# Performance work log

Hardware: AMD Instinct MI355X
Metric: run time of the kernel (lower is better)

Reference implementation:

```python
import jax, jax.numpy as jnp
import numpy as np

# Hardcoded hyperparameters from the torch module
E = 128   # n_embd
H = 4     # n_head
HS = 32   # head_size = n_embd // n_head
L = 4     # n_layer
T = 512   # block_size (full context)
V = 512   # vocab_size (quantization_levels)
B = 64    # batch
SCALE = 0.02  # init std per _init_weights


def _ln(x, g, b):
    mu = x.mean(-1, keepdims=True)
    var = ((x - mu) ** 2).mean(-1, keepdims=True)
    return (x - mu) / jnp.sqrt(var + 1e-5) * g + b


def setup_inputs() -> dict:
    key = jax.random.key(0)
    ks = jax.random.split(key, 24)
    rn = lambda k, shape: SCALE * jax.random.normal(k, shape, dtype=jnp.float32)
    return {
        "idx": jax.random.randint(ks[0], (B, T), 0, V),
        "tok_emb": rn(ks[1], (V, E)),
        "pos_emb": rn(ks[2], (T, E)),
        # per-head projections, stacked over layers and heads: x[...,E] @ wq[l,h] -> [...,HS]
        "wq": rn(ks[3], (L, H, E, HS)),
        "wk": rn(ks[4], (L, H, E, HS)),
        "wv": rn(ks[5], (L, H, E, HS)),
        "w_proj": rn(ks[6], (L, E, E)),   # torch Linear weight layout [out, in]
        "b_proj": jnp.zeros((L, E), jnp.float32),
        "ln1_g": jnp.ones((L, E), jnp.float32),
        "ln1_b": jnp.zeros((L, E), jnp.float32),
        "ln2_g": jnp.ones((L, E), jnp.float32),
        "ln2_b": jnp.zeros((L, E), jnp.float32),
        "w1": rn(ks[7], (L, 4 * E, E)),
        "b1": jnp.zeros((L, 4 * E), jnp.float32),
        "w2": rn(ks[8], (L, E, 4 * E)),
        "b2": jnp.zeros((L, E), jnp.float32),
        "lnf_g": jnp.ones((E,), jnp.float32),
        "lnf_b": jnp.zeros((E,), jnp.float32),
        "w_head": rn(ks[9], (V, E)),
        "b_head": jnp.zeros((V,), jnp.float32),
    }


def reference(idx, tok_emb, pos_emb, wq, wk, wv, w_proj, b_proj,
              ln1_g, ln1_b, ln2_g, ln2_b, w1, b1, w2, b2,
              lnf_g, lnf_b, w_head, b_head):
    Bv, Tv = idx.shape
    x = tok_emb[idx] + pos_emb[None, :Tv, :]          # [B,T,E]
    causal = jnp.tril(jnp.ones((Tv, Tv), dtype=bool))
    for l in range(L):
        h = _ln(x, ln1_g[l], ln1_b[l])
        q = jnp.einsum('bte,hed->bhtd', h, wq[l])     # [B,H,T,HS]
        k = jnp.einsum('bte,hed->bhtd', h, wk[l])
        v = jnp.einsum('bte,hed->bhtd', h, wv[l])
        s = jnp.einsum('bhtd,bhsd->bhts', q, k) * (HS ** -0.5)
        s = jnp.where(causal, s, -jnp.inf)
        a = jax.nn.softmax(s, axis=-1)
        o = jnp.einsum('bhts,bhsd->bhtd', a, v)       # [B,H,T,HS]
        o = o.transpose(0, 2, 1, 3).reshape(Bv, Tv, E)  # concat heads
        x = x + o @ w_proj[l].T + b_proj[l]
        h = _ln(x, ln2_g[l], ln2_b[l])
        x = x + jax.nn.gelu(h @ w1[l].T + b1[l], approximate=False) @ w2[l].T + b2[l]
    x = _ln(x, lnf_g, lnf_b)
    logits = x @ w_head.T + b_head                    # [B,T,V]
    return logits
```

## Files before the change

kernel.cpp:

```cpp
#include <hip/hip_runtime.h>

typedef __bf16 bf16x8 __attribute__((ext_vector_type(8)));
typedef __bf16 bf16x2 __attribute__((ext_vector_type(2)));
typedef float f32x4 __attribute__((ext_vector_type(4)));

constexpr int E_ = 128, H_ = 4, HS_ = 32, L_ = 4, T_ = 512, V_ = 512, B_ = 64;
constexpr int M_ = B_ * T_;

__device__ __forceinline__ float b2f(ushort u) {
    return __uint_as_float(((uint)u) << 16);
}
__device__ __forceinline__ ushort f2b(float f) {
    uint x = __float_as_uint(f);
    uint r = (x + 0x7fffu + ((x >> 16) & 1u)) >> 16;
    return (ushort)r;
}
__device__ __forceinline__ uint packbf(float a, float b) {
    bf16x2 t; t[0] = (__bf16)a; t[1] = (__bf16)b;
    return __builtin_bit_cast(uint, t);
}

constexpr int kNSeg = 19;
constexpr int kOffs[kNSeg + 1] = {
    0, 65536, 131072, 196608, 262144, 327680, 393216, 393728, 394240, 394752,
    395264, 395776, 657920, 659968, 922112, 922624, 922752, 922880, 988416, 988928
};
constexpr int kTotal = 988928;

struct SrcPtrs { const void* p[kNSeg]; };

__global__ __launch_bounds__(256) void k_convert(SrcPtrs sp, ushort* __restrict__ arena) {
    int gid = blockIdx.x * 256 + threadIdx.x;
    if (gid >= kTotal) return;
    bool isf32 = (((const uint*)sp.p[7])[0] == 0x3F800000u);
    int s = 0;
    #pragma unroll
    for (int i = 1; i < kNSeg; i++) if (gid >= kOffs[i]) s = i;
    int local = gid - kOffs[s];
    ushort v;
    if (isf32) v = f2b(((const float*)sp.p[s])[local]);
    else       v = ((const ushort*)sp.p[s])[local];
    arena[gid] = v;
}

__global__ void k_prep_qkv(const ushort* __restrict__ wq, const ushort* __restrict__ wk,
                           const ushort* __restrict__ wv, ushort* __restrict__ wt) {
    int gid = blockIdx.x * 256 + threadIdx.x;
    if (gid >= L_ * 384 * E_) return;
    int e = gid & 127;
    int n = (gid >> 7) % 384;
    int l = gid / (384 * E_);
    int part = n >> 7, within = n & 127, hh = within >> 5, d = within & 31;
    const ushort* src = part == 0 ? wq : (part == 1 ? wk : wv);
    wt[gid] = src[(((size_t)(l * H_ + hh) * E_) + e) * HS_ + d];
}

__global__ __launch_bounds__(256) void k_embed_ln(const int* __restrict__ idx,
                                                  const ushort* __restrict__ tok,
                                                  const ushort* __restrict__ pos,
                                                  const ushort* __restrict__ g,
                                                  const ushort* __restrict__ beta,
                                                  float* __restrict__ x, ushort* __restrict__ h) {
    int wave = threadIdx.x >> 6, lane = threadIdx.x & 63;
    int row = blockIdx.x * 4 + wave;
    int t = row & (T_ - 1);
    int id = idx[row];
    float v0 = b2f(tok[id * E_ + lane])      + b2f(pos[t * E_ + lane]);
    float v1 = b2f(tok[id * E_ + lane + 64]) + b2f(pos[t * E_ + lane + 64]);
    size_t o = (size_t)row * E_;
    x[o + lane] = v0; x[o + lane + 64] = v1;
    float s = v0 + v1;
    #pragma unroll
    for (int m = 32; m; m >>= 1) s += __shfl_xor(s, m, 64);
    float mu = s * (1.0f / 128.0f);
    float d0 = v0 - mu, d1 = v1 - mu;
    float ss = d0 * d0 + d1 * d1;
    #pragma unroll
    for (int m = 32; m; m >>= 1) ss += __shfl_xor(ss, m, 64);
    float rstd = rsqrtf(ss * (1.0f / 128.0f) + 1e-5f);
    h[o + lane]      = f2b(d0 * rstd * b2f(g[lane])      + b2f(beta[lane]));
    h[o + lane + 64] = f2b(d1 * rstd * b2f(g[lane + 64]) + b2f(beta[lane + 64]));
}

template<int EPI>
__global__ __launch_bounds__(256) void k_gemm(const ushort* __restrict__ A, const ushort* __restrict__ W,
                                              const ushort* __restrict__ bias, void* __restrict__ outp,
                                              void* __restrict__ outp2,
                                              const ushort* __restrict__ lng, const ushort* __restrict__ lnb,
                                              const uint* __restrict__ dtraw, int K, int lda, int ldc) {
    int wid = threadIdx.x >> 6, lane = threadIdx.x & 63;
    int wr = wid >> 1, wc = wid & 1;
    int bm = blockIdx.x, bn = blockIdx.y;
    int r16 = lane & 15, kq = lane >> 4;
    const ushort* Abase = A + (size_t)(bm * 128 + wr * 64 + r16) * lda + kq * 8;
    const ushort* Wbase = W + (size_t)(bn * 128 + wc * 64 + r16) * K + kq * 8;
    bool f32out = false;
    if constexpr (EPI == 1) f32out = (dtraw[0] == 0x3F800000u);
    f32x4 acc[4][4];
    #pragma unroll
    for (int i = 0; i < 4; i++)
        #pragma unroll
        for (int j = 0; j < 4; j++) acc[i][j] = (f32x4)0.0f;
    for (int k0 = 0; k0 < K; k0 += 32) {
        bf16x8 af[4], wf[4];
        #pragma unroll
        for (int mi = 0; mi < 4; mi++)
            af[mi] = *(const bf16x8*)(Abase + (size_t)mi * 16 * lda + k0);
        #pragma unroll
        for (int ni = 0; ni < 4; ni++)
            wf[ni] = *(const bf16x8*)(Wbase + (size_t)ni * 16 * K + k0);
        #pragma unroll
        for (int mi = 0; mi < 4; mi++)
            #pragma unroll
            for (int ni = 0; ni < 4; ni++)
                acc[mi][ni] = __builtin_amdgcn_mfma_f32_16x16x32_bf16(af[mi], wf[ni], acc[mi][ni], 0, 0, 0);
    }
    int orow0 = bm * 128 + wr * 64 + kq * 4;
    int ocol0 = bn * 128 + wc * 64 + r16;
    if constexpr (EPI == 5) {
        __shared__ float lnS[2][128], lnQ[2][128];
        float*  xg = (float*)outp;
        ushort* hg = (ushort*)outp2;
        #pragma unroll
        for (int ni = 0; ni < 4; ni++) {
            int col = ocol0 + ni * 16;
            float bv = b2f(bias[col]);
            #pragma unroll
            for (int mi = 0; mi < 4; mi++) {
                #pragma unroll
                for (int e = 0; e < 4; e++) {
                    size_t gi = (size_t)(orow0 + mi * 16 + e) * 128 + col;
                    float xv = xg[gi] + acc[mi][ni][e] + bv;
                    xg[gi] = xv;
                    acc[mi][ni][e] = xv;
                }
            }
        }
        #pragma unroll
        for (int mi = 0; mi < 4; mi++) {
            #pragma unroll
            for (int e = 0; e < 4; e++) {
                float s = 0.f, q = 0.f;
                #pragma unroll
                for (int ni = 0; ni < 4; ni++) { float v = acc[mi][ni][e]; s += v; q += v * v; }
                #pragma unroll
                for (int mk = 1; mk < 16; mk <<= 1) {
                    s += __shfl_xor(s, mk, 64); q += __shfl_xor(q, mk, 64);
                }
                if (r16 == 0) {
                    int lrow = wr * 64 + mi * 16 + kq * 4 + e;
                    lnS[wc][lrow] = s; lnQ[wc][lrow] = q;
                }
            }
        }
        __syncthreads();
        float gc[4], bc[4];
        #pragma unroll
        for (int ni = 0; ni < 4; ni++) {
            int col = ocol0 + ni * 16;
            gc[ni] = b2f(lng[col]); bc[ni] = b2f(lnb[col]);
        }
        #pragma unroll
        for (int mi = 0; mi < 4; mi++) {
            #pragma unroll
            for (int e = 0; e < 4; e++) {
                int lrow = wr * 64 + mi * 16 + kq * 4 + e;
                float tot = lnS[0][lrow] + lnS[1][lrow];
                float tq  = lnQ[0][lrow] + lnQ[1][lrow];
                float mu  = tot * (1.0f / 128.0f);
                float var = tq * (1.0f / 128.0f) - mu * mu;
                float rstd = rsqrtf(var + 1e-5f);
                size_t grow = (size_t)(bm * 128 + lrow) * 128;
                #pragma unroll
                for (int ni = 0; ni < 4; ni++) {
                    int col = ocol0 + ni * 16;
                    hg[grow + col] = f2b((acc[mi][ni][e] - mu) * rstd * gc[ni] + bc[ni]);
                }
            }
        }
        return;
    }
    if constexpr (EPI == 4) {
        if (bn == 2) {
            ushort* vt = (ushort*)outp2;
            #pragma unroll
            for (int mi = 0; mi < 4; mi++) {
                int row0 = orow0 + mi * 16;
                int bb = row0 >> 9, tt = row0 & 511;
                #pragma unroll
                for (int ni = 0; ni < 4; ni++) {
                    int vd = (ocol0 - 256) + ni * 16;
                    int hh = vd >> 5, dd = vd & 31;
                    ushort4 pk;
                    pk.x = f2b(acc[mi][ni][0]); pk.y = f2b(acc[mi][ni][1]);
                    pk.z = f2b(acc[mi][ni][2]); pk.w = f2b(acc[mi][ni][3]);
                    *(ushort4*)(vt + (((size_t)(bb * 4 + hh) * 32 + dd) << 9) + tt) = pk;
                }
            }
            return;
        }
    }
    #pragma unroll
    for (int mi = 0; mi < 4; mi++) {
        #pragma unroll
        for (int ni = 0; ni < 4; ni++) {
            int col = ocol0 + ni * 16;
            float bv = 0.0f;
            if constexpr (EPI == 1 || EPI == 2) bv = b2f(bias[col]);
            #pragma unroll
            for (int e = 0; e < 4; e++) {
                int row = orow0 + mi * 16 + e;
                float v = acc[mi][ni][e] + bv;
                if constexpr (EPI == 2) v = 0.5f * v * (1.0f + erff(v * 0.70710678118f));
                if constexpr (EPI == 1) {
                    if (f32out) ((float*)outp)[(size_t)row * ldc + col] = v;
                    else        ((ushort*)outp)[(size_t)row * ldc + col] = f2b(v);
                } else {
                    ((ushort*)outp)[(size_t)row * ldc + col] = f2b(v);
                }
            }
        }
    }
}

constexpr float SC_ = 0.2550348637f;

__device__ __forceinline__ bf16x8 scale8(bf16x8 v, float s) {
    bf16x8 r;
    #pragma unroll
    for (int i = 0; i < 8; i++) r[i] = (__bf16)((float)v[i] * s);
    return r;
}

__device__ __forceinline__ bf16x8 relayoutP(const float* p, int r16, int g) {
    uint pk00 = packbf(p[0], p[1]), pk01 = packbf(p[2], p[3]);
    uint pk10 = packbf(p[4], p[5]), pk11 = packbf(p[6], p[7]);
    int ga = ((g & 1) << 5) + r16;
    int gb = ga + 16;
    uint A0 = (uint)__shfl((int)pk00, ga), A1 = (uint)__shfl((int)pk01, ga);
    uint C0 = (uint)__shfl((int)pk00, gb), C1 = (uint)__shfl((int)pk01, gb);
    uint B0 = (uint)__shfl((int)pk10, ga), B1 = (uint)__shfl((int)pk11, ga);
    uint D0 = (uint)__shfl((int)pk10, gb), D1 = (uint)__shfl((int)pk11, gb);
    bool hi2 = g >= 2;
    uint4 pr;
    pr.x = hi2 ? B0 : A0; pr.y = hi2 ? B1 : A1;
    pr.z = hi2 ? D0 : C0; pr.w = hi2 ? D1 : C1;
    return __builtin_bit_cast(bf16x8, pr);
}

__global__ __launch_bounds__(256) void k_attn_proj(const ushort* __restrict__ qk,
                                                   const ushort* __restrict__ vt,
                                                   const ushort* __restrict__ wproj,
                                                   const ushort* __restrict__ bproj,
                                                   const ushort* __restrict__ lng,
                                                   const ushort* __restrict__ lnb,
                                                   float* __restrict__ x,
                                                   ushort* __restrict__ h) {
    __shared__ ushort olds[16 * 128];
    __shared__ float lnS[4][16], lnQ[4][16];
    int lane = threadIdx.x & 63, w = threadIdx.x >> 6;
    int r16 = lane & 15, g = lane >> 4;
    int bid = blockIdx.x;
    int b = (bid & 7) * 8 + ((bid >> 3) >> 5);
    int i = (bid >> 3) & 31;
    int qbase = i * 16, qmax = qbase + 15, myq = qbase + r16;
    const ushort* qkbase = qk + (size_t)b * 512 * 256;
    bf16x8 qf = scale8(*(const bf16x8*)(qkbase + (size_t)(qbase + r16) * 256 + w * 32 + g * 8), SC_);
    const ushort* kptr = qkbase + 128 + w * 32 + g * 8;
    const ushort* vbase = vt + ((size_t)(b * 4 + w) * 32) * 512;

    f32x4 o0 = (f32x4)0.0f, o1 = (f32x4)0.0f;
    float ps = 0.0f;
    for (int j0 = 0; j0 <= qmax; j0 += 32) {
        bf16x8 kf0 = *(const bf16x8*)(kptr + (size_t)(j0 + r16) * 256);
        bf16x8 kf1 = *(const bf16x8*)(kptr + (size_t)(j0 + 16 + r16) * 256);
        bf16x8 vf0 = *(const bf16x8*)(vbase + (size_t)r16 * 512 + j0 + g * 8);
        bf16x8 vf1 = *(const bf16x8*)(vbase + (size_t)(16 + r16) * 512 + j0 + g * 8);
        f32x4 s0 = __builtin_amdgcn_mfma_f32_16x16x32_bf16(kf0, qf, (f32x4)0.0f, 0, 0, 0);
        f32x4 s1 = __builtin_amdgcn_mfma_f32_16x16x32_bf16(kf1, qf, (f32x4)0.0f, 0, 0, 0);
        float p[8];
        #pragma unroll
        for (int e = 0; e < 4; e++) {
            int ja = j0 + 4 * g + e;
            p[e]     = (ja      <= myq) ? exp2f(s0[e]) : 0.0f;
            p[4 + e] = (ja + 16 <= myq) ? exp2f(s1[e]) : 0.0f;
            ps += p[e] + p[4 + e];
        }
        bf16x8 pf = relayoutP(p, r16, g);
        o0 = __builtin_amdgcn_mfma_f32_16x16x32_bf16(vf0, pf, o0, 0, 0, 0);
        o1 = __builtin_amdgcn_mfma_f32_16x16x32_bf16(vf1, pf, o1, 0, 0, 0);
    }
    ps += __shfl_xor(ps, 16, 64);
    ps += __shfl_xor(ps, 32, 64);
    float inv = 1.0f / ps;
    {
        int base = r16 * 256 + w * 64 + g * 8;
        int sw = (r16 & 7) << 4;
        uint2 pk0, pk1;
        pk0.x = packbf(o0[0] * inv, o0[1] * inv); pk0.y = packbf(o0[2] * inv, o0[3] * inv);
        pk1.x = packbf(o1[0] * inv, o1[1] * inv); pk1.y = packbf(o1[2] * inv, o1[3] * inv);
        *(uint2*)((char*)olds + (base ^ sw))        = pk0;
        *(uint2*)((char*)olds + ((base + 32) ^ sw)) = pk1;
    }
    __syncthreads();
    f32x4 a0 = (f32x4)0.0f, a1 = (f32x4)0.0f;
    const ushort* wp0 = wproj + (size_t)(w * 32 + r16) * 128 + g * 8;
    const ushort* wp1 = wp0 + (size_t)16 * 128;
    #pragma unroll
    for (int kk = 0; kk < 4; kk++) {
        int abyte = (r16 * 256 + kk * 64 + g * 16) ^ ((r16 & 7) << 4);
        bf16x8 af = *(const bf16x8*)((const char*)olds + abyte);
        bf16x8 w0 = *(const bf16x8*)(wp0 + kk * 32);
        bf16x8 w1 = *(const bf16x8*)(wp1 + kk * 32);
        a0 = __builtin_amdgcn_mfma_f32_16x16x32_bf16(af, w0, a0, 0, 0, 0);
        a1 = __builtin_amdgcn_mfma_f32_16x16x32_bf16(af, w1, a1, 0, 0, 0);
    }
    int col0 = w * 32 + r16, col1 = col0 + 16;
    float bv0 = b2f(bproj[col0]), bv1 = b2f(bproj[col1]);
    float xv0[4], xv1[4];
    #pragma unroll
    for (int e = 0; e < 4; e++) {
        size_t gi = (size_t)(b * 512 + qbase + g * 4 + e) * 128;
        float v0 = x[gi + col0] + a0[e] + bv0;
        float v1 = x[gi + col1] + a1[e] + bv1;
        x[gi + col0] = v0; x[gi + col1] = v1;
        xv0[e] = v0; xv1[e] = v1;
    }
    #pragma unroll
    for (int e = 0; e < 4; e++) {
        float s = xv0[e] + xv1[e];
        float q = xv0[e] * xv0[e] + xv1[e] * xv1[e];
        #pragma unroll
        for (int mk = 1; mk < 16; mk <<= 1) {
            s += __shfl_xor(s, mk, 64); q += __shfl_xor(q, mk, 64);
        }
        if (r16 == 0) { lnS[w][g * 4 + e] = s; lnQ[w][g * 4 + e] = q; }
    }
    __syncthreads();
    float g0 = b2f(lng[col0]), g1 = b2f(lng[col1]);
    float be0 = b2f(lnb[col0]), be1 = b2f(lnb[col1]);
    #pragma unroll
    for (int e = 0; e < 4; e++) {
        int q = g * 4 + e;
        float tot = lnS[0][q] + lnS[1][q] + lnS[2][q] + lnS[3][q];
        float tq  = lnQ[0][q] + lnQ[1][q] + lnQ[2][q] + lnQ[3][q];
        float mu  = tot * (1.0f / 128.0f);
        float var = tq * (1.0f / 128.0f) - mu * mu;
        float rstd = rsqrtf(var + 1e-5f);
        size_t gr = (size_t)(b * 512 + qbase + q) * 128;
        h[gr + col0] = f2b((xv0[e] - mu) * rstd * g0 + be0);
        h[gr + col1] = f2b((xv1[e] - mu) * rstd * g1 + be1);
    }
}

extern "C" void kernel_launch(void* const* d_in, const int* in_sizes, int n_in,
                              void* d_out, int out_size, void* d_ws, size_t ws_size,
                              hipStream_t stream) {
    const int* idx = (const int*)d_in[0];

    char* ws = (char*)d_ws;
    float*  x     = (float*) (ws + 0);
    ushort* h     = (ushort*)(ws + (16u << 20));
    ushort* wqkvt = (ushort*)(ws + (24u << 20));
    ushort* arena = (ushort*)(ws + (25u << 20));

    ushort* qkv = (ushort*)d_out;
    ushort* vt  = (ushort*)d_out + (12u << 20);
    ushort* mid = (ushort*)d_out;

    const ushort* tok    = arena + kOffs[0];
    const ushort* pos    = arena + kOffs[1];
    const ushort* wqp    = arena + kOffs[2];
    const ushort* wkp    = arena + kOffs[3];
    const ushort* wvp    = arena + kOffs[4];
    const ushort* w_proj = arena + kOffs[5];
    const ushort* b_proj = arena + kOffs[6];
    const ushort* ln1_g  = arena + kOffs[7];
    const ushort* ln1_b  = arena + kOffs[8];
    const ushort* ln2_g  = arena + kOffs[9];
    const ushort* ln2_b  = arena + kOffs[10];
    const ushort* w1     = arena + kOffs[11];
    const ushort* b1     = arena + kOffs[12];
    const ushort* w2     = arena + kOffs[13];
    const ushort* b2     = arena + kOffs[14];
    const ushort* lnf_g  = arena + kOffs[15];
    const ushort* lnf_b  = arena + kOffs[16];
    const ushort* w_head = arena + kOffs[17];
    const ushort* b_head = arena + kOffs[18];

    SrcPtrs sp;
    for (int i = 0; i < kNSeg; i++) sp.p[i] = d_in[i + 1];
    k_convert<<<(kTotal + 255) / 256, 256, 0, stream>>>(sp, arena);

    k_prep_qkv<<<768, 256, 0, stream>>>(wqp, wkp, wvp, wqkvt);
    k_embed_ln<<<M_ / 4, 256, 0, stream>>>(idx, tok, pos, ln1_g, ln1_b, x, h);
    for (int l = 0; l < L_; l++) {
        const ushort* ng = (l < 3) ? (ln1_g + (l + 1) * E_) : lnf_g;
        const ushort* nb = (l < 3) ? (ln1_b + (l + 1) * E_) : lnf_b;
        k_gemm<4><<<dim3(M_ / 128, 3), 256, 0, stream>>>(h, wqkvt + (size_t)l * 384 * E_, nullptr,
                                                         qkv, vt, nullptr, nullptr, nullptr, 128, 128, 256);
        k_attn_proj<<<2048, 256, 0, stream>>>(qkv, vt, w_proj + (size_t)l * E_ * E_, b_proj + l * E_,
                                              ln2_g + l * E_, ln2_b + l * E_, x, h);
        k_gemm<2><<<dim3(M_ / 128, 4), 256, 0, stream>>>(h, w1 + (size_t)l * 4 * E_ * E_, b1 + l * 4 * E_,
                                                         mid, nullptr, nullptr, nullptr, nullptr, 128, 128, 512);
        k_gemm<5><<<dim3(M_ / 128, 1), 256, 0, stream>>>(mid, w2 + (size_t)l * E_ * 4 * E_, b2 + l * E_,
                                                         x, h, ng, nb, nullptr, 512, 512, 128);
    }
    k_gemm<1><<<dim3(M_ / 128, 4), 256, 0, stream>>>(h, w_head, b_head, d_out, nullptr,
                                                     nullptr, nullptr, (const uint*)d_in[8], 128, 128, 512);
}
```

Baseline: 550.7 us.

## Pair complementary causal query tiles per attention block for load balance

Each attention block now handles two 16-row query tiles, p and 31-p, so every block does about the same causal work, and the grid is halved. K/V fragments loaded once per key step are shared by both tiles, which reduces redundant global loads. The projection and layernorm epilogue is extended to 32 rows. This costs more registers per thread and gives fewer blocks to fill the device.

```diff
diff --git a/kernel.cpp b/kernel.cpp
--- a/kernel.cpp
+++ b/kernel.cpp
@@ -256,100 +256,141 @@
                                                    const ushort* __restrict__ lnb,
                                                    float* __restrict__ x,
                                                    ushort* __restrict__ h) {
-    __shared__ ushort olds[16 * 128];
-    __shared__ float lnS[4][16], lnQ[4][16];
+    __shared__ ushort olds[32 * 128];
+    __shared__ float lnS[4][32], lnQ[4][32];
     int lane = threadIdx.x & 63, w = threadIdx.x >> 6;
     int r16 = lane & 15, g = lane >> 4;
     int bid = blockIdx.x;
-    int b = (bid & 7) * 8 + ((bid >> 3) >> 5);
-    int i = (bid >> 3) & 31;
-    int qbase = i * 16, qmax = qbase + 15, myq = qbase + r16;
+    int b = (bid & 7) * 8 + (bid >> 7);
+    int p = (bid >> 3) & 15;
+    int qbaseA = p * 16, qbaseB = (31 - p) * 16;
+    int myqA = qbaseA + r16, myqB = qbaseB + r16;
+    int qmaxA = qbaseA + 15, qmaxB = qbaseB + 15;
     const ushort* qkbase = qk + (size_t)b * 512 * 256;
-    bf16x8 qf = scale8(*(const bf16x8*)(qkbase + (size_t)(qbase + r16) * 256 + w * 32 + g * 8), SC_);
+    bf16x8 qfA = scale8(*(const bf16x8*)(qkbase + (size_t)(qbaseA + r16) * 256 + w * 32 + g * 8), SC_);
+    bf16x8 qfB = scale8(*(const bf16x8*)(qkbase + (size_t)(qbaseB + r16) * 256 + w * 32 + g * 8), SC_);
     const ushort* kptr = qkbase + 128 + w * 32 + g * 8;
     const ushort* vbase = vt + ((size_t)(b * 4 + w) * 32) * 512;
 
-    f32x4 o0 = (f32x4)0.0f, o1 = (f32x4)0.0f;
-    float ps = 0.0f;
-    for (int j0 = 0; j0 <= qmax; j0 += 32) {
+    f32x4 oA0 = (f32x4)0.0f, oA1 = (f32x4)0.0f, oB0 = (f32x4)0.0f, oB1 = (f32x4)0.0f;
+    float psA = 0.0f, psB = 0.0f;
+    for (int j0 = 0; j0 <= qmaxB; j0 += 32) {
         bf16x8 kf0 = *(const bf16x8*)(kptr + (size_t)(j0 + r16) * 256);
         bf16x8 kf1 = *(const bf16x8*)(kptr + (size_t)(j0 + 16 + r16) * 256);
         bf16x8 vf0 = *(const bf16x8*)(vbase + (size_t)r16 * 512 + j0 + g * 8);
         bf16x8 vf1 = *(const bf16x8*)(vbase + (size_t)(16 + r16) * 512 + j0 + g * 8);
-        f32x4 s0 = __builtin_amdgcn_mfma_f32_16x16x32_bf16(kf0, qf, (f32x4)0.0f, 0, 0, 0);
-        f32x4 s1 = __builtin_amdgcn_mfma_f32_16x16x32_bf16(kf1, qf, (f32x4)0.0f, 0, 0, 0);
-        float p[8];
-        #pragma unroll
-        for (int e = 0; e < 4; e++) {
-            int ja = j0 + 4 * g + e;
-            p[e]     = (ja      <= myq) ? exp2f(s0[e]) : 0.0f;
-            p[4 + e] = (ja + 16 <= myq) ? exp2f(s1[e]) : 0.0f;
-            ps += p[e] + p[4 + e];
-        }
-        bf16x8 pf = relayoutP(p, r16, g);
-        o0 = __builtin_amdgcn_mfma_f32_16x16x32_bf16(vf0, pf, o0, 0, 0, 0);
-        o1 = __builtin_amdgcn_mfma_f32_16x16x32_bf16(vf1, pf, o1, 0, 0, 0);
-    }
-    ps += __shfl_xor(ps, 16, 64);
-    ps += __shfl_xor(ps, 32, 64);
-    float inv = 1.0f / ps;
+        {
+            f32x4 s0 = __builtin_amdgcn_mfma_f32_16x16x32_bf16(kf0, qfB, (f32x4)0.0f, 0, 0, 0);
+            f32x4 s1 = __builtin_amdgcn_mfma_f32_16x16x32_bf16(kf1, qfB, (f32x4)0.0f, 0, 0, 0);
+            float pv[8];
+            #pragma unroll
+            for (int e = 0; e < 4; e++) {
+                int ja = j0 + 4 * g + e;
+                pv[e]     = (ja      <= myqB) ? exp2f(s0[e]) : 0.0f;
+                pv[4 + e] = (ja + 16 <= myqB) ? exp2f(s1[e]) : 0.0f;
+                psB += pv[e] + pv[4 + e];
+            }
+            bf16x8 pf = relayoutP(pv, r16, g);
+            oB0 = __builtin_amdgcn_mfma_f32_16x16x32_bf16(vf0, pf, oB0, 0, 0, 0);
+            oB1 = __builtin_amdgcn_mfma_f32_16x16x32_bf16(vf1, pf, oB1, 0, 0, 0);
+        }
+        if (j0 <= qmaxA) {
+            f32x4 s0 = __builtin_amdgcn_mfma_f32_16x16x32_bf16(kf0, qfA, (f32x4)0.0f, 0, 0, 0);
+            f32x4 s1 = __builtin_amdgcn_mfma_f32_16x16x32_bf16(kf1, qfA, (f32x4)0.0f, 0, 0, 0);
+            float pv[8];
+            #pragma unroll
+            for (int e = 0; e < 4; e++) {
+                int ja = j0 + 4 * g + e;
+                pv[e]     = (ja      <= myqA) ? exp2f(s0[e]) : 0.0f;
+                pv[4 + e] = (ja + 16 <= myqA) ? exp2f(s1[e]) : 0.0f;
+                psA += pv[e] + pv[4 + e];
+            }
+            bf16x8 pf = relayoutP(pv, r16, g);
+            oA0 = __builtin_amdgcn_mfma_f32_16x16x32_bf16(vf0, pf, oA0, 0, 0, 0);
+            oA1 = __builtin_amdgcn_mfma_f32_16x16x32_bf16(vf1, pf, oA1, 0, 0, 0);
+        }
+    }
+    psA += __shfl_xor(psA, 16, 64); psA += __shfl_xor(psA, 32, 64);
+    psB += __shfl_xor(psB, 16, 64); psB += __shfl_xor(psB, 32, 64);
     {
-        int base = r16 * 256 + w * 64 + g * 8;
+        float invA = 1.0f / psA, invB = 1.0f / psB;
         int sw = (r16 & 7) << 4;
-        uint2 pk0, pk1;
-        pk0.x = packbf(o0[0] * inv, o0[1] * inv); pk0.y = packbf(o0[2] * inv, o0[3] * inv);
-        pk1.x = packbf(o1[0] * inv, o1[1] * inv); pk1.y = packbf(o1[2] * inv, o1[3] * inv);
-        *(uint2*)((char*)olds + (base ^ sw))        = pk0;
-        *(uint2*)((char*)olds + ((base + 32) ^ sw)) = pk1;
+        int baseA = r16 * 256 + w * 64 + g * 8;
+        int baseB = (16 + r16) * 256 + w * 64 + g * 8;
+        uint2 a0, a1, b0, b1;
+        a0.x = packbf(oA0[0] * invA, oA0[1] * invA); a0.y = packbf(oA0[2] * invA, oA0[3] * invA);
+        a1.x = packbf(oA1[0] * invA, oA1[1] * invA); a1.y = packbf(oA1[2] * invA, oA1[3] * invA);
+        b0.x = packbf(oB0[0] * invB, oB0[1] * invB); b0.y = packbf(oB0[2] * invB, oB0[3] * invB);
+        b1.x = packbf(oB1[0] * invB, oB1[1] * invB); b1.y = packbf(oB1[2] * invB, oB1[3] * invB);
+        *(uint2*)((char*)olds + (baseA ^ sw))        = a0;
+        *(uint2*)((char*)olds + ((baseA + 32) ^ sw)) = a1;
+        *(uint2*)((char*)olds + (baseB ^ sw))        = b0;
+        *(uint2*)((char*)olds + ((baseB + 32) ^ sw)) = b1;
     }
     __syncthreads();
-    f32x4 a0 = (f32x4)0.0f, a1 = (f32x4)0.0f;
+    f32x4 acc[2][2];
+    acc[0][0] = (f32x4)0.0f; acc[0][1] = (f32x4)0.0f;
+    acc[1][0] = (f32x4)0.0f; acc[1][1] = (f32x4)0.0f;
     const ushort* wp0 = wproj + (size_t)(w * 32 + r16) * 128 + g * 8;
     const ushort* wp1 = wp0 + (size_t)16 * 128;
     #pragma unroll
     for (int kk = 0; kk < 4; kk++) {
-        int abyte = (r16 * 256 + kk * 64 + g * 16) ^ ((r16 & 7) << 4);
-        bf16x8 af = *(const bf16x8*)((const char*)olds + abyte);
         bf16x8 w0 = *(const bf16x8*)(wp0 + kk * 32);
         bf16x8 w1 = *(const bf16x8*)(wp1 + kk * 32);
-        a0 = __builtin_amdgcn_mfma_f32_16x16x32_bf16(af, w0, a0, 0, 0, 0);
-        a1 = __builtin_amdgcn_mfma_f32_16x16x32_bf16(af, w1, a1, 0, 0, 0);
+        #pragma unroll
+        for (int mi = 0; mi < 2; mi++) {
+            int abyte = ((mi * 16 + r16) * 256 + kk * 64 + g * 16) ^ ((r16 & 7) << 4);
+            bf16x8 af = *(const bf16x8*)((const char*)olds + abyte);
+            acc[mi][0] = __builtin_amdgcn_mfma_f32_16x16x32_bf16(af, w0, acc[mi][0], 0, 0, 0);
+            acc[mi][1] = __builtin_amdgcn_mfma_f32_16x16x32_bf16(af, w1, acc[mi][1], 0, 0, 0);
+        }
     }
     int col0 = w * 32 + r16, col1 = col0 + 16;
     float bv0 = b2f(bproj[col0]), bv1 = b2f(bproj[col1]);
-    float xv0[4], xv1[4];
-    #pragma unroll
-    for (int e = 0; e < 4; e++) {
-        size_t gi = (size_t)(b * 512 + qbase + g * 4 + e) * 128;
-        float v0 = x[gi + col0] + a0[e] + bv0;
-        float v1 = x[gi + col1] + a1[e] + bv1;
-        x[gi + col0] = v0; x[gi + col1] = v1;
-        xv0[e] = v0; xv1[e] = v1;
-    }
-    #pragma unroll
-    for (int e = 0; e < 4; e++) {
-        float s = xv0[e] + xv1[e];
-        float q = xv0[e] * xv0[e] + xv1[e] * xv1[e];
-        #pragma unroll
-        for (int mk = 1; mk < 16; mk <<= 1) {
-            s += __shfl_xor(s, mk, 64); q += __shfl_xor(q, mk, 64);
-        }
-        if (r16 == 0) { lnS[w][g * 4 + e] = s; lnQ[w][g * 4 + e] = q; }
+    float xv[2][2][4];
+    #pragma unroll
+    for (int mi = 0; mi < 2; mi++) {
+        int qb = mi == 0 ? qbaseA : qbaseB;
+        #pragma unroll
+        for (int e = 0; e < 4; e++) {
+            size_t gi = (size_t)(b * 512 + qb + g * 4 + e) * 128;
+            float v0 = x[gi + col0] + acc[mi][0][e] + bv0;
+            float v1 = x[gi + col1] + acc[mi][1][e] + bv1;
+            x[gi + col0] = v0; x[gi + col1] = v1;
+            xv[mi][0][e] = v0; xv[mi][1][e] = v1;
+        }
+    }
+    #pragma unroll
+    for (int mi = 0; mi < 2; mi++) {
+        #pragma unroll
+        for (int e = 0; e < 4; e++) {
+            float s = xv[mi][0][e] + xv[mi][1][e];
+            float q = xv[mi][0][e] * xv[mi][0][e] + xv[mi][1][e] * xv[mi][1][e];
+            #pragma unroll
+            for (int mk = 1; mk < 16; mk <<= 1) {
+                s += __shfl_xor(s, mk, 64); q += __shfl_xor(q, mk, 64);
+            }
+            if (r16 == 0) { lnS[w][mi * 16 + g * 4 + e] = s; lnQ[w][mi * 16 + g * 4 + e] = q; }
+        }
     }
     __syncthreads();
     float g0 = b2f(lng[col0]), g1 = b2f(lng[col1]);
     float be0 = b2f(lnb[col0]), be1 = b2f(lnb[col1]);
     #pragma unroll
-    for (int e = 0; e < 4; e++) {
-        int q = g * 4 + e;
-        float tot = lnS[0][q] + lnS[1][q] + lnS[2][q] + lnS[3][q];
-        float tq  = lnQ[0][q] + lnQ[1][q] + lnQ[2][q] + lnQ[3][q];
-        float mu  = tot * (1.0f / 128.0f);
-        float var = tq * (1.0f / 128.0f) - mu * mu;
-        float rstd = rsqrtf(var + 1e-5f);
-        size_t gr = (size_t)(b * 512 + qbase + q) * 128;
-        h[gr + col0] = f2b((xv0[e] - mu) * rstd * g0 + be0);
-        h[gr + col1] = f2b((xv1[e] - mu) * rstd * g1 + be1);
+    for (int mi = 0; mi < 2; mi++) {
+        int qb = mi == 0 ? qbaseA : qbaseB;
+        #pragma unroll
+        for (int e = 0; e < 4; e++) {
+            int lr = mi * 16 + g * 4 + e;
+            float tot = lnS[0][lr] + lnS[1][lr] + lnS[2][lr] + lnS[3][lr];
+            float tq  = lnQ[0][lr] + lnQ[1][lr] + lnQ[2][lr] + lnQ[3][lr];
+            float mu  = tot * (1.0f / 128.0f);
+            float var = tq * (1.0f / 128.0f) - mu * mu;
+            float rstd = rsqrtf(var + 1e-5f);
+            size_t gr = (size_t)(b * 512 + qb + g * 4 + e) * 128;
+            h[gr + col0] = f2b((xv[mi][0][e] - mu) * rstd * g0 + be0);
+            h[gr + col1] = f2b((xv[mi][1][e] - mu) * rstd * g1 + be1);
+        }
     }
 }
 
@@ -399,7 +440,7 @@
         const ushort* nb = (l < 3) ? (ln1_b + (l + 1) * E_) : lnf_b;
         k_gemm<4><<<dim3(M_ / 128, 3), 256, 0, stream>>>(h, wqkvt + (size_t)l * 384 * E_, nullptr,
                                                          qkv, vt, nullptr, nullptr, nullptr, 128, 128, 256);
-        k_attn_proj<<<2048, 256, 0, stream>>>(qkv, vt, w_proj + (size_t)l * E_ * E_, b_proj + l * E_,
+        k_attn_proj<<<1024, 256, 0, stream>>>(qkv, vt, w_proj + (size_t)l * E_ * E_, b_proj + l * E_,
                                               ln2_g + l * E_, ln2_b + l * E_, x, h);
         k_gemm<2><<<dim3(M_ / 128, 4), 256, 0, stream>>>(h, w1 + (size_t)l * 4 * E_ * E_, b1 + l * 4 * E_,
                                                          mid, nullptr, nullptr, nullptr, nullptr, 128, 128, 512);
```

After: 500.3 us. 1.1x faster.
